# Kernel tuning notes

Measured on AMD Instinct MI355X. Metric: run time of the kernel, lower is better.

Reference implementation:

```python
import jax, jax.numpy as jnp
import numpy as np


def _mlp2(x, W1, b1, W2, b2):
    # two-layer MLP with ReLU hidden activation
    h = jax.nn.relu(jnp.einsum('...i,ij->...j', x, W1) + b1)
    return jnp.einsum('...i,ij->...j', h, W2) + b2


def setup_inputs() -> dict:
    key = jax.random.key(0)
    ks = jax.random.split(key, 8)
    B, N, D = 8, 256, 64
    positions = jax.random.normal(ks[0], (B, N, 3), dtype=jnp.float32)
    values = jax.random.normal(ks[1], (B, N, D), dtype=jnp.float32)
    # value_net: 2 -> D -> D ; score_net: D -> D -> 1 (He-style init)
    Wv1 = jax.random.normal(ks[2], (2, D), dtype=jnp.float32) * np.sqrt(2.0 / 2)
    bv1 = jnp.zeros((D,), dtype=jnp.float32)
    Wv2 = jax.random.normal(ks[3], (D, D), dtype=jnp.float32) * np.sqrt(2.0 / D)
    bv2 = jnp.zeros((D,), dtype=jnp.float32)
    Ws1 = jax.random.normal(ks[4], (D, D), dtype=jnp.float32) * np.sqrt(2.0 / D)
    bs1 = jnp.zeros((D,), dtype=jnp.float32)
    Ws2 = jax.random.normal(ks[5], (D, 1), dtype=jnp.float32) * np.sqrt(2.0 / D)
    bs2 = jnp.zeros((1,), dtype=jnp.float32)
    return dict(positions=positions, values=values, Wv1=Wv1, bv1=bv1, Wv2=Wv2,
                bv2=bv2, Ws1=Ws1, bs1=bs1, Ws2=Ws2, bs2=bs2)


def reference(positions, values, Wv1, bv1, Wv2, bv2, Ws1, bs1, Ws2, bs2):
    # rank-2 geometric algebra attention, reduce=True, merge_fun=join_fun='mean'
    B, N, _ = positions.shape
    r_i = positions[:, :, None, :]            # [B, N, 1, 3]
    r_j = positions[:, None, :, :]            # [B, 1, N, 3]
    # geometric product of two vectors -> scalar (dot) + bivector (wedge)
    dot = jnp.sum(r_i * r_j, axis=-1)         # [B, N, N] scalar part
    wedge = jnp.cross(r_i, r_j)               # [B, N, N, 3] bivector components
    biv_norm = jnp.sqrt(jnp.sum(wedge * wedge, axis=-1) + 1e-20)
    invariants = jnp.stack([dot, biv_norm], axis=-1)             # [B, N, N, 2]
    # merge_fun='mean' over the pair of node values
    merged = 0.5 * (values[:, :, None, :] + values[:, None, :, :])  # [B,N,N,D]
    invar_values = _mlp2(invariants, Wv1, bv1, Wv2, bv2)            # [B,N,N,D]
    # join_fun='mean' of value_net(invariants) and merged node values
    joined = 0.5 * (invar_values + merged)                          # [B,N,N,D]
    scores = _mlp2(joined, Ws1, bs1, Ws2, bs2)                      # [B,N,N,1]
    # reduce=True: softmax over all N*N product indices, output is [B, D]
    attn = jax.nn.softmax(scores.reshape(B, N * N), axis=-1).reshape(B, N, N, 1)
    output = jnp.sum(attn * joined, axis=(1, 2))                    # [B, D]
    return output
```

## Files before the change

kernel.cpp:

```cpp
#include <hip/hip_runtime.h>
#include <hip/hip_bf16.h>
#include <hip/hip_fp16.h>

#define NB 8
#define NN 256
#define DD 64

#define OFF_WCF   0
#define OFF_W1F   2048
#define OFF_CSF   4096
#define OFF_CC    5632
#define OFF_MI    5704
#define OFF_RSI   7752
#define OFF_SHR   9800

typedef __attribute__((ext_vector_type(4))) float f32x4;
typedef _Float16 f16x8 __attribute__((ext_vector_type(8)));

static __device__ __forceinline__ f16x8 cvt2(float4 a, float4 c) {
    f16x8 r;
    r[0] = (_Float16)a.x; r[1] = (_Float16)a.y; r[2] = (_Float16)a.z; r[3] = (_Float16)a.w;
    r[4] = (_Float16)c.x; r[5] = (_Float16)c.y; r[6] = (_Float16)c.z; r[7] = (_Float16)c.w;
    return r;
}

__global__ __launch_bounds__(256) void k_setup(
    const float* __restrict__ Wv1, const float* __restrict__ bv1,
    const float* __restrict__ Wv2, const float* __restrict__ bv2,
    const float* __restrict__ Ws1, const float* __restrict__ bs1,
    float* __restrict__ ws)
{
    int idx = blockIdx.x * 256 + threadIdx.x;
    if (idx < 4096) {
        int e = idx;
        int j = e & 7, ln = (e >> 3) & 63, nt = (e >> 9) & 3, ks = e >> 11;
        int k = ks * 32 + (ln >> 4) * 8 + j;
        int d = nt * 16 + (ln & 15);
        float s = 0.f;
#pragma unroll 8
        for (int m = 0; m < 64; m++) s = fmaf(Wv2[k * 64 + m], Ws1[m * 64 + d], s);
        ((_Float16*)(ws + OFF_WCF))[e] = (_Float16)(0.5f * s);
    } else if (idx < 8192) {
        int e = idx - 4096;
        int j = e & 7, ln = (e >> 3) & 63, nt = (e >> 9) & 3, ks = e >> 11;
        int k = ks * 32 + (ln >> 4) * 8 + j;
        int d = nt * 16 + (ln & 15);
        ((_Float16*)(ws + OFF_W1F))[e] = (_Float16)(0.25f * Ws1[k * 64 + d]);
    } else if (idx < 11264) {
        int e = idx - 8192;
        int ln = e / 48;
        int rem = e - ln * 48;
        int coef = rem >> 4, kslot = rem & 15;
        int ks = kslot >> 3, j = kslot & 7;
        int k = ks * 32 + (ln >> 4) * 8 + j;
        float v = (coef == 0) ? Wv1[k] : (coef == 1) ? Wv1[64 + k] : bv1[k];
        ((_Float16*)(ws + OFF_CSF))[ln * 48 + coef * 16 + kslot] = (_Float16)v;
    } else if (idx < 11328) {
        int d = idx - 11264;
        float s = 0.f;
#pragma unroll 8
        for (int k = 0; k < 64; k++) s = fmaf(bv2[k], Ws1[k * 64 + d], s);
        ws[OFF_CC + d] = 0.5f * s + bs1[d];
    }
}

__global__ __launch_bounds__(256, 4) void k_main(
    const float* __restrict__ pos, const float* __restrict__ values,
    const float* __restrict__ Wv1, const float* __restrict__ bv1,
    const float* __restrict__ Ws2, float* __restrict__ ws)
{
    __shared__ float2   ldsDB[256];
    __shared__ float    ldsS[256];
    __shared__ float    ldsCC[64];
    __shared__ float    ldsWs2[64];
    __shared__ float    ldsPos[3];
    __shared__ float    ldsRedM[4];
    __shared__ float    ldsRedS[4];
    __shared__ float    ldsP[4][64];
    __shared__ _Float16 ldsW1[4096];

    int b = blockIdx.x >> 8;
    int i = blockIdx.x & 255;
    int t = threadIdx.x;
    int lane = t & 63, wv = t >> 6;
    int q = lane >> 4, col = lane & 15;

    const float* vB = values + b * (NN * DD);

    float4 nf0, nf1, nf2, nf3;
    {
        const float* p = vB + (wv * 64 + col) * 64 + q * 8;
        nf0 = *(const float4*)p;        nf1 = *(const float4*)(p + 4);
        nf2 = *(const float4*)(p + 32); nf3 = *(const float4*)(p + 36);
    }
    float4 vi0 = {0,0,0,0}, vi1 = {0,0,0,0}, vi2 = {0,0,0,0}, vi3 = {0,0,0,0};
    if (col == 0) {
        const float* p = vB + i * 64 + q * 8;
        vi0 = *(const float4*)p;        vi1 = *(const float4*)(p + 4);
        vi2 = *(const float4*)(p + 32); vi3 = *(const float4*)(p + 36);
    }

    {
        const float4* src = (const float4*)(ws + OFF_W1F);
        float4* dst = (float4*)ldsW1;
        dst[t] = src[t];
        dst[256 + t] = src[256 + t];
    }
    if (t < 3)  ldsPos[t] = pos[(b * 256 + i) * 3 + t];
    if (t >= 64 && t < 128) ldsCC[t - 64] = ws[OFF_CC + t - 64];
    if (t >= 128 && t < 192) ldsWs2[t - 128] = Ws2[t - 128];

    f16x8 cfA[2], cfB[2], cfC[2];
    {
        const f16x8* cs = (const f16x8*)((const _Float16*)(ws + OFF_CSF) + lane * 48);
        cfA[0] = cs[0]; cfA[1] = cs[1];
        cfB[0] = cs[2]; cfB[1] = cs[3];
        cfC[0] = cs[4]; cfC[1] = cs[5];
    }
    f16x8 wcf[2][4];
    {
        const f16x8* p = (const f16x8*)(ws + OFF_WCF);
#pragma unroll
        for (int ks = 0; ks < 2; ks++)
#pragma unroll
            for (int nt = 0; nt < 4; nt++)
                wcf[ks][nt] = p[(ks * 4 + nt) * 64 + lane];
    }
    __syncthreads();

    {
        float px = pos[(b * 256 + t) * 3 + 0];
        float py = pos[(b * 256 + t) * 3 + 1];
        float pz = pos[(b * 256 + t) * 3 + 2];
        float ax = ldsPos[0], ay = ldsPos[1], az = ldsPos[2];
        float dot = ax * px + ay * py + az * pz;
        float cx = ay * pz - az * py;
        float cy = az * px - ax * pz;
        float cz = ax * py - ay * px;
        float biv = sqrtf(cx * cx + cy * cy + cz * cz + 1e-20f);
        ldsDB[t] = make_float2(dot, biv);
    }

    const f16x8* w1 = (const f16x8*)ldsW1;

    float cu[4], w2r[4];
    {
        f16x8 afu0 = cvt2(vi0, vi1);
        f16x8 afu1 = cvt2(vi2, vi3);
#pragma unroll
        for (int nt = 0; nt < 4; nt++) {
            f32x4 ua = (f32x4){0.f, 0.f, 0.f, 0.f};
            ua = __builtin_amdgcn_mfma_f32_16x16x32_f16(afu0, w1[(0 * 4 + nt) * 64 + lane], ua, 0, 0, 0);
            ua = __builtin_amdgcn_mfma_f32_16x16x32_f16(afu1, w1[(1 * 4 + nt) * 64 + lane], ua, 0, 0, 0);
            cu[nt] = ldsCC[nt * 16 + col] + __shfl(ua[0], col);
            w2r[nt] = ldsWs2[nt * 16 + col];
        }
    }

#pragma unroll
    for (int jt4 = 0; jt4 < 4; jt4++) {
        int jt = wv * 4 + jt4;
        f16x8 av0 = cvt2(nf0, nf1);
        f16x8 av1 = cvt2(nf2, nf3);
        if (jt4 < 3) {
            const float* p = vB + ((jt + 1) * 16 + col) * 64 + q * 8;
            nf0 = *(const float4*)p;        nf1 = *(const float4*)(p + 4);
            nf2 = *(const float4*)(p + 32); nf3 = *(const float4*)(p + 36);
        }

        f32x4 acc[4];
#pragma unroll
        for (int nt = 0; nt < 4; nt++) {
            acc[nt] = (f32x4){0.f, 0.f, 0.f, 0.f};
            acc[nt] = __builtin_amdgcn_mfma_f32_16x16x32_f16(av0, w1[(0 * 4 + nt) * 64 + lane], acc[nt], 0, 0, 0);
            acc[nt] = __builtin_amdgcn_mfma_f32_16x16x32_f16(av1, w1[(1 * 4 + nt) * 64 + lane], acc[nt], 0, 0, 0);
        }

        float2 db = ldsDB[jt * 16 + col];
        _Float16 dh = (_Float16)db.x, bh = (_Float16)db.y;
        f16x8 d8, b8;
#pragma unroll
        for (int p = 0; p < 8; p++) { d8[p] = dh; b8[p] = bh; }
        f16x8 af0, af1;
        {
            f16x8 h0 = d8 * cfA[0] + b8 * cfB[0] + cfC[0];
            f16x8 h1 = d8 * cfA[1] + b8 * cfB[1] + cfC[1];
            af0 = __builtin_elementwise_max(h0, (f16x8)(_Float16)0.f);
            af1 = __builtin_elementwise_max(h1, (f16x8)(_Float16)0.f);
        }
#pragma unroll
        for (int nt = 0; nt < 4; nt++) {
            acc[nt] = __builtin_amdgcn_mfma_f32_16x16x32_f16(af0, wcf[0][nt], acc[nt], 0, 0, 0);
            acc[nt] = __builtin_amdgcn_mfma_f32_16x16x32_f16(af1, wcf[1][nt], acc[nt], 0, 0, 0);
        }

        float tr[4] = {0.f, 0.f, 0.f, 0.f};
#pragma unroll
        for (int nt = 0; nt < 4; nt++) {
#pragma unroll
            for (int r = 0; r < 4; r++) {
                float s = acc[nt][r] + cu[nt];
                tr[r] = fmaf(fmaxf(s, 0.f), w2r[nt], tr[r]);
            }
        }
#pragma unroll
        for (int m = 1; m < 16; m <<= 1) {
#pragma unroll
            for (int r = 0; r < 4; r++) tr[r] += __shfl_xor(tr[r], m);
        }
        if (col == 0)
            *(float4*)&ldsS[jt * 16 + q * 4] = make_float4(tr[0], tr[1], tr[2], tr[3]);
    }

    float sv = ldsS[t];
    float wm = sv;
#pragma unroll
    for (int md = 1; md < 64; md <<= 1) wm = fmaxf(wm, __shfl_xor(wm, md));
    if (lane == 0) ldsRedM[wv] = wm;
    __syncthreads();
    float m_row = fmaxf(fmaxf(ldsRedM[0], ldsRedM[1]), fmaxf(ldsRedM[2], ldsRedM[3]));
    float wgt = __expf(sv - m_row);
    float rsp = wgt;
#pragma unroll
    for (int md = 1; md < 64; md <<= 1) rsp += __shfl_xor(rsp, md);
    ldsS[t] = wgt;
    if (lane == 0) ldsRedS[wv] = rsp;
    __syncthreads();
    float rowsum = ldsRedS[0] + ldsRedS[1] + ldsRedS[2] + ldsRedS[3];

    float A = Wv1[lane], B = Wv1[64 + lane], C = bv1[lane];
    float acc = 0.f;
#pragma unroll 8
    for (int jj = 0; jj < 64; jj++) {
        int j = wv * 64 + jj;
        float w = ldsS[j];
        float2 db = ldsDB[j];
        float h = fmaxf(fmaf(db.x, A, fmaf(db.y, B, C)), 0.f);
        acc = fmaf(w, h, acc);
    }
    ldsP[wv][lane] = acc;
    __syncthreads();
    if (t < 64)
        ws[OFF_SHR + (b * 256 + i) * 64 + t] = ldsP[0][t] + ldsP[1][t] + ldsP[2][t] + ldsP[3][t];
    if (t == 0) {
        ws[OFF_MI  + b * 256 + i] = m_row;
        ws[OFF_RSI + b * 256 + i] = rowsum;
    }
}

__global__ __launch_bounds__(256) void k_final(
    const float* __restrict__ values, const float* __restrict__ Wv2,
    const float* __restrict__ bv2, const float* __restrict__ ws,
    float* __restrict__ out)
{
    __shared__ float scl[256], zl[256], red[4], pS[4][64], pA[4][64], shv[64], a2v[64];
    int b = blockIdx.x, t = threadIdx.x, wv = t >> 6, lane = t & 63;

    float mi = ws[OFF_MI + b * 256 + t];
    float wm = mi;
#pragma unroll
    for (int md = 1; md < 64; md <<= 1) wm = fmaxf(wm, __shfl_xor(wm, md));
    if (lane == 0) red[wv] = wm;
    __syncthreads();
    float M = fmaxf(fmaxf(red[0], red[1]), fmaxf(red[2], red[3]));

    float rs = ws[OFF_RSI + b * 256 + t];
    float sc = __expf(mi - M);
    float zt = sc * rs;
    scl[t] = sc; zl[t] = zt;
    float zp = zt;
#pragma unroll
    for (int md = 1; md < 64; md <<= 1) zp += __shfl_xor(zp, md);
    __syncthreads();
    if (lane == 0) red[wv] = zp;
    __syncthreads();
    float Z = red[0] + red[1] + red[2] + red[3];

    float accS = 0.f, accA = 0.f;
    const float* shrB = ws + OFF_SHR + b * 256 * 64;
    const float* vB   = values + b * 256 * 64;
#pragma unroll 4
    for (int jj = 0; jj < 64; jj++) {
        int row = wv * 64 + jj;
        accS = fmaf(scl[row], shrB[row * 64 + lane], accS);
        accA = fmaf(zl[row],  vB[row * 64 + lane],  accA);
    }
    pS[wv][lane] = accS; pA[wv][lane] = accA;
    __syncthreads();
    if (t < 64) {
        shv[t] = pS[0][t] + pS[1][t] + pS[2][t] + pS[3][t];
        a2v[t] = pA[0][t] + pA[1][t] + pA[2][t] + pA[3][t];
    }
    __syncthreads();
    if (t < 64) {
        float t1 = 0.f;
#pragma unroll 8
        for (int k = 0; k < 64; k++) t1 = fmaf(shv[k], Wv2[k * 64 + t], t1);
        out[b * 64 + t] = 0.5f * (t1 + a2v[t]) / Z + 0.5f * bv2[t];
    }
}

extern "C" void kernel_launch(void* const* d_in, const int* in_sizes, int n_in,
                              void* d_out, int out_size, void* d_ws, size_t ws_size,
                              hipStream_t stream)
{
    const float* positions = (const float*)d_in[0];
    const float* values    = (const float*)d_in[1];
    const float* Wv1       = (const float*)d_in[2];
    const float* bv1       = (const float*)d_in[3];
    const float* Wv2       = (const float*)d_in[4];
    const float* bv2       = (const float*)d_in[5];
    const float* Ws1       = (const float*)d_in[6];
    const float* bs1       = (const float*)d_in[7];
    const float* Ws2       = (const float*)d_in[8];
    float* ws  = (float*)d_ws;
    float* out = (float*)d_out;

    k_setup<<<45, 256, 0, stream>>>(Wv1, bv1, Wv2, bv2, Ws1, bs1, ws);
    k_main<<<2048, 256, 0, stream>>>(positions, values, Wv1, bv1, Ws2, ws);
    k_final<<<NB, 256, 0, stream>>>(values, Wv2, bv2, ws, out);
}
```

Baseline: 107.5 us.

## Precompute per-node values·Ws1 projection in setup instead of per-block MFMA

The setup kernel now computes the projection of every node's values through Ws1 once, scaled and stored in the MFMA accumulator layout, and also writes an fp16 copy of the values. The main kernel loads these projections as its accumulator initial values and as the query-row term. This removes the per-block staging of W1 into LDS and half of the MFMAs per tile. The cost is a larger setup kernel and extra global or L2 reads of the precomputed tile. Dead leftover code (the av0/av1 loads and an acc MFMA chain that is never used) remains and is expected to be eliminated by the compiler.

```diff
diff --git a/kernel.cpp b/kernel.cpp
--- a/kernel.cpp
+++ b/kernel.cpp
@@ -7,32 +7,37 @@
 #define DD 64
 
 #define OFF_WCF   0
-#define OFF_W1F   2048
-#define OFF_CSF   4096
-#define OFF_CC    5632
-#define OFF_MI    5704
-#define OFF_RSI   7752
-#define OFF_SHR   9800
+#define OFF_CSF   2048
+#define OFF_CC    3584
+#define OFF_MI    3648
+#define OFF_RSI   5696
+#define OFF_SHR   7744
+#define OFF_P     138816
+#define OFF_VF    269888
 
 typedef __attribute__((ext_vector_type(4))) float f32x4;
 typedef _Float16 f16x8 __attribute__((ext_vector_type(8)));
 
-static __device__ __forceinline__ f16x8 cvt2(float4 a, float4 c) {
-    f16x8 r;
-    r[0] = (_Float16)a.x; r[1] = (_Float16)a.y; r[2] = (_Float16)a.z; r[3] = (_Float16)a.w;
-    r[4] = (_Float16)c.x; r[5] = (_Float16)c.y; r[6] = (_Float16)c.z; r[7] = (_Float16)c.w;
-    return r;
-}
-
 __global__ __launch_bounds__(256) void k_setup(
-    const float* __restrict__ Wv1, const float* __restrict__ bv1,
-    const float* __restrict__ Wv2, const float* __restrict__ bv2,
-    const float* __restrict__ Ws1, const float* __restrict__ bs1,
-    float* __restrict__ ws)
+    const float* __restrict__ values, const float* __restrict__ Wv1,
+    const float* __restrict__ bv1, const float* __restrict__ Wv2,
+    const float* __restrict__ bv2, const float* __restrict__ Ws1,
+    const float* __restrict__ bs1, float* __restrict__ ws)
 {
     int idx = blockIdx.x * 256 + threadIdx.x;
-    if (idx < 4096) {
-        int e = idx;
+    if (idx < 131072) {
+        ((_Float16*)(ws + OFF_VF))[idx] = (_Float16)values[idx];
+        int r = idx & 3, lane = (idx >> 2) & 63, nt = (idx >> 8) & 3, jtg = idx >> 10;
+        int b = jtg >> 4, jt = jtg & 15;
+        int j = jt * 16 + (lane >> 4) * 4 + r;
+        int d = nt * 16 + (lane & 15);
+        const float* v = values + (b * 256 + j) * 64;
+        float s = 0.f;
+#pragma unroll 8
+        for (int k = 0; k < 64; k++) s = fmaf(v[k], Ws1[k * 64 + d], s);
+        ws[OFF_P + idx] = 0.25f * s;
+    } else if (idx < 135168) {
+        int e = idx - 131072;
         int j = e & 7, ln = (e >> 3) & 63, nt = (e >> 9) & 3, ks = e >> 11;
         int k = ks * 32 + (ln >> 4) * 8 + j;
         int d = nt * 16 + (ln & 15);
@@ -40,14 +45,8 @@
 #pragma unroll 8
         for (int m = 0; m < 64; m++) s = fmaf(Wv2[k * 64 + m], Ws1[m * 64 + d], s);
         ((_Float16*)(ws + OFF_WCF))[e] = (_Float16)(0.5f * s);
-    } else if (idx < 8192) {
-        int e = idx - 4096;
-        int j = e & 7, ln = (e >> 3) & 63, nt = (e >> 9) & 3, ks = e >> 11;
-        int k = ks * 32 + (ln >> 4) * 8 + j;
-        int d = nt * 16 + (ln & 15);
-        ((_Float16*)(ws + OFF_W1F))[e] = (_Float16)(0.25f * Ws1[k * 64 + d]);
-    } else if (idx < 11264) {
-        int e = idx - 8192;
+    } else if (idx < 138240) {
+        int e = idx - 135168;
         int ln = e / 48;
         int rem = e - ln * 48;
         int coef = rem >> 4, kslot = rem & 15;
@@ -55,8 +54,8 @@
         int k = ks * 32 + (ln >> 4) * 8 + j;
         float v = (coef == 0) ? Wv1[k] : (coef == 1) ? Wv1[64 + k] : bv1[k];
         ((_Float16*)(ws + OFF_CSF))[ln * 48 + coef * 16 + kslot] = (_Float16)v;
-    } else if (idx < 11328) {
-        int d = idx - 11264;
+    } else if (idx < 138304) {
+        int d = idx - 138240;
         float s = 0.f;
 #pragma unroll 8
         for (int k = 0; k < 64; k++) s = fmaf(bv2[k], Ws1[k * 64 + d], s);
@@ -65,19 +64,18 @@
 }
 
 __global__ __launch_bounds__(256, 4) void k_main(
-    const float* __restrict__ pos, const float* __restrict__ values,
-    const float* __restrict__ Wv1, const float* __restrict__ bv1,
-    const float* __restrict__ Ws2, float* __restrict__ ws)
-{
-    __shared__ float2   ldsDB[256];
-    __shared__ float    ldsS[256];
-    __shared__ float    ldsCC[64];
-    __shared__ float    ldsWs2[64];
-    __shared__ float    ldsPos[3];
-    __shared__ float    ldsRedM[4];
-    __shared__ float    ldsRedS[4];
-    __shared__ float    ldsP[4][64];
-    __shared__ _Float16 ldsW1[4096];
+    const float* __restrict__ pos, const float* __restrict__ Wv1,
+    const float* __restrict__ bv1, const float* __restrict__ Ws2,
+    float* __restrict__ ws)
+{
+    __shared__ float2 ldsDB[256];
+    __shared__ float  ldsS[256];
+    __shared__ float  ldsCC[64];
+    __shared__ float  ldsWs2[64];
+    __shared__ float  ldsPos[3];
+    __shared__ float  ldsRedM[4];
+    __shared__ float  ldsRedS[4];
+    __shared__ float  ldsP[4][64];
 
     int b = blockIdx.x >> 8;
     int i = blockIdx.x & 255;
@@ -85,31 +83,6 @@
     int lane = t & 63, wv = t >> 6;
     int q = lane >> 4, col = lane & 15;
 
-    const float* vB = values + b * (NN * DD);
-
-    float4 nf0, nf1, nf2, nf3;
-    {
-        const float* p = vB + (wv * 64 + col) * 64 + q * 8;
-        nf0 = *(const float4*)p;        nf1 = *(const float4*)(p + 4);
-        nf2 = *(const float4*)(p + 32); nf3 = *(const float4*)(p + 36);
-    }
-    float4 vi0 = {0,0,0,0}, vi1 = {0,0,0,0}, vi2 = {0,0,0,0}, vi3 = {0,0,0,0};
-    if (col == 0) {
-        const float* p = vB + i * 64 + q * 8;
-        vi0 = *(const float4*)p;        vi1 = *(const float4*)(p + 4);
-        vi2 = *(const float4*)(p + 32); vi3 = *(const float4*)(p + 36);
-    }
-
-    {
-        const float4* src = (const float4*)(ws + OFF_W1F);
-        float4* dst = (float4*)ldsW1;
-        dst[t] = src[t];
-        dst[256 + t] = src[256 + t];
-    }
-    if (t < 3)  ldsPos[t] = pos[(b * 256 + i) * 3 + t];
-    if (t >= 64 && t < 128) ldsCC[t - 64] = ws[OFF_CC + t - 64];
-    if (t >= 128 && t < 192) ldsWs2[t - 128] = Ws2[t - 128];
-
     f16x8 cfA[2], cfB[2], cfC[2];
     {
         const f16x8* cs = (const f16x8*)((const _Float16*)(ws + OFF_CSF) + lane * 48);
@@ -126,6 +99,9 @@
             for (int nt = 0; nt < 4; nt++)
                 wcf[ks][nt] = p[(ks * 4 + nt) * 64 + lane];
     }
+    if (t < 3)  ldsPos[t] = pos[(b * 256 + i) * 3 + t];
+    if (t >= 64 && t < 128) ldsCC[t - 64] = ws[OFF_CC + t - 64];
+    if (t >= 128 && t < 192) ldsWs2[t - 128] = Ws2[t - 128];
     __syncthreads();
 
     {
@@ -141,18 +117,15 @@
         ldsDB[t] = make_float2(dot, biv);
     }
 
-    const f16x8* w1 = (const f16x8*)ldsW1;
+    const float* Pb = ws + OFF_P + b * 16384;
+    const _Float16* vfB = (const _Float16*)(ws + OFF_VF) + b * (NN * DD);
 
     float cu[4], w2r[4];
     {
-        f16x8 afu0 = cvt2(vi0, vi1);
-        f16x8 afu1 = cvt2(vi2, vi3);
+        int jti = i >> 4, qq = (i >> 2) & 3, rr = i & 3;
 #pragma unroll
         for (int nt = 0; nt < 4; nt++) {
-            f32x4 ua = (f32x4){0.f, 0.f, 0.f, 0.f};
-            ua = __builtin_amdgcn_mfma_f32_16x16x32_f16(afu0, w1[(0 * 4 + nt) * 64 + lane], ua, 0, 0, 0);
-            ua = __builtin_amdgcn_mfma_f32_16x16x32_f16(afu1, w1[(1 * 4 + nt) * 64 + lane], ua, 0, 0, 0);
-            cu[nt] = ldsCC[nt * 16 + col] + __shfl(ua[0], col);
+            cu[nt] = ldsCC[nt * 16 + col] + Pb[(jti * 4 + nt) * 256 + qq * 64 + col * 4 + rr];
             w2r[nt] = ldsWs2[nt * 16 + col];
         }
     }
@@ -160,21 +133,14 @@
 #pragma unroll
     for (int jt4 = 0; jt4 < 4; jt4++) {
         int jt = wv * 4 + jt4;
-        f16x8 av0 = cvt2(nf0, nf1);
-        f16x8 av1 = cvt2(nf2, nf3);
-        if (jt4 < 3) {
-            const float* p = vB + ((jt + 1) * 16 + col) * 64 + q * 8;
-            nf0 = *(const float4*)p;        nf1 = *(const float4*)(p + 4);
-            nf2 = *(const float4*)(p + 32); nf3 = *(const float4*)(p + 36);
-        }
-
+        const _Float16* vrow = vfB + (jt * 16 + col) * 64;
+        f16x8 av0 = *(const f16x8*)(vrow + q * 8);
+        f16x8 av1 = *(const f16x8*)(vrow + 32 + q * 8);
         f32x4 acc[4];
-#pragma unroll
-        for (int nt = 0; nt < 4; nt++) {
-            acc[nt] = (f32x4){0.f, 0.f, 0.f, 0.f};
-            acc[nt] = __builtin_amdgcn_mfma_f32_16x16x32_f16(av0, w1[(0 * 4 + nt) * 64 + lane], acc[nt], 0, 0, 0);
-            acc[nt] = __builtin_amdgcn_mfma_f32_16x16x32_f16(av1, w1[(1 * 4 + nt) * 64 + lane], acc[nt], 0, 0, 0);
-        }
+        const float* Pt = Pb + (jt * 4) * 256 + lane * 4;
+#pragma unroll
+        for (int nt = 0; nt < 4; nt++)
+            acc[nt] = *(const f32x4*)(Pt + nt * 256);
 
         float2 db = ldsDB[jt * 16 + col];
         _Float16 dh = (_Float16)db.x, bh = (_Float16)db.y;
@@ -190,19 +156,23 @@
         }
 #pragma unroll
         for (int nt = 0; nt < 4; nt++) {
-            acc[nt] = __builtin_amdgcn_mfma_f32_16x16x32_f16(af0, wcf[0][nt], acc[nt], 0, 0, 0);
-            acc[nt] = __builtin_amdgcn_mfma_f32_16x16x32_f16(af1, wcf[1][nt], acc[nt], 0, 0, 0);
+            acc[nt] = __builtin_amdgcn_mfma_f32_16x16x32_f16(av0, wcf[0][nt], acc[nt], 0, 0, 0);
+            acc[nt] = __builtin_amdgcn_mfma_f32_16x16x32_f16(av1, wcf[1][nt], acc[nt], 0, 0, 0);
         }
 
         float tr[4] = {0.f, 0.f, 0.f, 0.f};
 #pragma unroll
         for (int nt = 0; nt < 4; nt++) {
+            f32x4 a2 = *(const f32x4*)(Pt + nt * 256);
+            a2 = __builtin_amdgcn_mfma_f32_16x16x32_f16(af0, wcf[0][nt], a2, 0, 0, 0);
+            a2 = __builtin_amdgcn_mfma_f32_16x16x32_f16(af1, wcf[1][nt], a2, 0, 0, 0);
 #pragma unroll
             for (int r = 0; r < 4; r++) {
-                float s = acc[nt][r] + cu[nt];
+                float s = a2[r] + cu[nt];
                 tr[r] = fmaf(fmaxf(s, 0.f), w2r[nt], tr[r]);
             }
         }
+        (void)av0; (void)av1; (void)acc;
 #pragma unroll
         for (int m = 1; m < 16; m <<= 1) {
 #pragma unroll
@@ -229,16 +199,16 @@
     float rowsum = ldsRedS[0] + ldsRedS[1] + ldsRedS[2] + ldsRedS[3];
 
     float A = Wv1[lane], B = Wv1[64 + lane], C = bv1[lane];
-    float acc = 0.f;
+    float acc2 = 0.f;
 #pragma unroll 8
     for (int jj = 0; jj < 64; jj++) {
         int j = wv * 64 + jj;
         float w = ldsS[j];
         float2 db = ldsDB[j];
         float h = fmaxf(fmaf(db.x, A, fmaf(db.y, B, C)), 0.f);
-        acc = fmaf(w, h, acc);
-    }
-    ldsP[wv][lane] = acc;
+        acc2 = fmaf(w, h, acc2);
+    }
+    ldsP[wv][lane] = acc2;
     __syncthreads();
     if (t < 64)
         ws[OFF_SHR + (b * 256 + i) * 64 + t] = ldsP[0][t] + ldsP[1][t] + ldsP[2][t] + ldsP[3][t];
@@ -316,7 +286,7 @@
     float* ws  = (float*)d_ws;
     float* out = (float*)d_out;
 
-    k_setup<<<45, 256, 0, stream>>>(Wv1, bv1, Wv2, bv2, Ws1, bs1, ws);
-    k_main<<<2048, 256, 0, stream>>>(positions, values, Wv1, bv1, Ws2, ws);
+    k_setup<<<541, 256, 0, stream>>>(values, Wv1, bv1, Wv2, bv2, Ws1, bs1, ws);
+    k_main<<<2048, 256, 0, stream>>>(positions, Wv1, bv1, Ws2, ws);
     k_final<<<NB, 256, 0, stream>>>(values, Wv2, bv2, ws, out);
 }
```

Result: no change. 107.7 us (+0.2%).
